# Kernel optimization log

Measured on AMD Instinct MI355X. Metric: run time of the kernel, lower is better.

Reference implementation:

```python
import jax, jax.numpy as jnp
import numpy as np

S, B, G, P = 8, 8192, 512, 16
E, H, BOT = 64, 64, 1024

def setup_inputs() -> dict:
    key = jax.random.key(0)
    k = jax.random.split(key, 9)
    in_xy = jax.random.normal(k[0], (S, B, 2), dtype=jnp.float32)
    in_dxdy = jax.random.normal(k[1], (S, B, 2), dtype=jnp.float32)
    h_states = jax.random.normal(k[2], (1, B, H), dtype=jnp.float32)
    starts = jnp.arange(G, dtype=jnp.int64) * P
    seq_start_end = jnp.stack([starts, starts + P], axis=1)
    W_emb = jax.random.normal(k[3], (2, E), dtype=jnp.float32) / jnp.sqrt(2.0)
    b_emb = jnp.zeros((E,), dtype=jnp.float32)
    W1 = jax.random.normal(k[4], (E + H, H), dtype=jnp.float32) / jnp.sqrt(float(E + H))
    b1 = jnp.zeros((H,), dtype=jnp.float32)
    W2 = jax.random.normal(k[5], (H, BOT), dtype=jnp.float32) / jnp.sqrt(float(H))
    b2 = jnp.zeros((BOT,), dtype=jnp.float32)
    return {"in_xy": in_xy, "in_dxdy": in_dxdy, "h_states": h_states,
            "seq_start_end": seq_start_end, "W_emb": W_emb, "b_emb": b_emb,
            "W1": W1, "b1": b1, "W2": W2, "b2": b2}

def reference(in_xy, in_dxdy, h_states, seq_start_end, W_emb, b_emb, W1, b1, W2, b2):
    # Uniform group size: P = batch / num_groups (groups are contiguous).
    batch = in_xy.shape[1]
    g = seq_start_end.shape[0]
    p = batch // g
    end_pos = in_xy[-1].reshape(g, p, 2)            # (G,P,2)
    h = h_states.reshape(batch, -1).reshape(g, p, -1)  # (G,P,H)
    # torch semantics: row (i*P+j) of the pair matrix uses pos[j]-pos[i], hidden[j]
    rel = end_pos[:, None, :, :] - end_pos[:, :, None, :]  # (G,P_i,P_j,2)
    emb = rel @ W_emb + b_emb                              # (G,P,P,E)
    hj = jnp.broadcast_to(h[:, None, :, :], (g, p, p, h.shape[-1]))
    x = jnp.concatenate([emb, hj], axis=-1)                # (G,P,P,E+H)
    x = jax.nn.relu(x @ W1 + b1)
    x = jax.nn.relu(x @ W2 + b2)                           # (G,P,P,BOT)
    pool = jnp.max(x, axis=2)                              # max over j -> (G,P,BOT)
    return pool.reshape(batch, -1)
```

## Files before the change

### kernel.cpp

```cpp
#include <hip/hip_runtime.h>
#include <hip/hip_bf16.h>

typedef __attribute__((ext_vector_type(8))) short bf16x8;
typedef __attribute__((ext_vector_type(4))) float f32x4;

#define NB 8192
#define NS 8

__device__ __forceinline__ unsigned short f2bf(float f) {
  union { float f; unsigned int u; } v; v.f = f;
  unsigned int r = v.u + 0x7FFFu + ((v.u >> 16) & 1u);
  return (unsigned short)(r >> 16);
}

__global__ __launch_bounds__(256) void prep_kernel(
    const float* __restrict__ W2, const float* __restrict__ W_emb,
    const float* __restrict__ b_emb, const float* __restrict__ W1,
    unsigned short* __restrict__ w2f, float* __restrict__ wc,
    unsigned short* __restrict__ w1bf) {
  int tid = blockIdx.x * 256 + threadIdx.x;
  if (tid < 8192) {
    int lane = tid & 63;
    int ks = (tid >> 6) & 1;
    int nt = tid >> 7;
    int col = nt * 16 + (lane & 15);
    int k0 = ks * 32 + (lane >> 4) * 8;
    bf16x8 pk;
#pragma unroll
    for (int e = 0; e < 8; ++e)
      pk[e] = (short)f2bf(W2[(k0 + e) * 1024 + col]);
    *(bf16x8*)(w2f + tid * 8) = pk;
  } else if (tid < 8192 + 192) {
    int t2 = tid - 8192;
    int c = t2 >> 6, k = t2 & 63;
    float s = 0.f;
    for (int e = 0; e < 64; ++e) {
      float src = (c < 2) ? W_emb[c * 64 + e] : b_emb[e];
      s += src * W1[e * 64 + k];
    }
    wc[t2] = s;
  } else if (tid < 8192 + 192 + 512) {
    int q = tid - 8384;
    int lane = q & 63;
    int fr = q >> 6;
    int nt = fr >> 1, ks = fr & 1;
    int col = nt * 16 + (lane & 15);
    int e0 = ks * 32 + (lane >> 4) * 8;
    bf16x8 pk;
#pragma unroll
    for (int e = 0; e < 8; ++e)
      pk[e] = (short)f2bf(W1[(64 + e0 + e) * 64 + col]);
    *(bf16x8*)(w1bf + q * 8) = pk;
  }
}

__global__ __launch_bounds__(64) void hw_kernel(
    const float* __restrict__ h_states, const float* __restrict__ b1,
    const float* __restrict__ wc, const unsigned short* __restrict__ w1bf,
    float* __restrict__ hW) {
  const int lane = threadIdx.x;
  const int b = blockIdx.x;
  const int row = b * 16 + (lane & 15);
  const int k0 = (lane >> 4) * 8;
  const float* hp = h_states + row * 64 + k0;
  bf16x8 a0, a1;
#pragma unroll
  for (int e = 0; e < 8; ++e) {
    a0[e] = (short)f2bf(hp[e]);
    a1[e] = (short)f2bf(hp[e + 32]);
  }
#pragma unroll
  for (int nt = 0; nt < 4; ++nt) {
    bf16x8 bf0 = *(const bf16x8*)(w1bf + ((nt * 2 + 0) * 64 + lane) * 8);
    bf16x8 bf1 = *(const bf16x8*)(w1bf + ((nt * 2 + 1) * 64 + lane) * 8);
    f32x4 z = {0.f, 0.f, 0.f, 0.f};
    f32x4 acc = __builtin_amdgcn_mfma_f32_16x16x32_bf16(a0, bf0, z, 0, 0, 0);
    acc = __builtin_amdgcn_mfma_f32_16x16x32_bf16(a1, bf1, acc, 0, 0, 0);
    int col = nt * 16 + (lane & 15);
    float bb = b1[col] + wc[128 + col];
#pragma unroll
    for (int r = 0; r < 4; ++r)
      hW[(b * 16 + (lane >> 4) * 4 + r) * 64 + col] = acc[r] + bb;
  }
}

__global__ __launch_bounds__(256, 4) void pool_kernel(
    const float* __restrict__ in_xy, const float* __restrict__ b2,
    const unsigned short* __restrict__ w2f, const float* __restrict__ wc,
    const float* __restrict__ hW, float* __restrict__ out) {
  __shared__ bf16x8 Afrag[2048];
  __shared__ float exy[32];
  const int g = blockIdx.x >> 1;
  const int half = blockIdx.x & 1;
  const int t = threadIdx.x;
  const int lane = t & 63;
  const int wv = t >> 6;

  if (t < 32) {
    int p = t & 15;
    exy[t] = in_xy[((NS - 1) * NB + g * 16 + p) * 2 + (t >> 4)];
  }

  float b2v[8];
#pragma unroll
  for (int u = 0; u < 8; ++u)
    b2v[u] = b2[half * 512 + wv * 128 + u * 16 + (lane & 15)];

  const int i = t & 15;
  const int kc = (t >> 4) & 3;
  const int ks = (t >> 6) & 1;
  const int k0 = ks * 32 + kc * 8;
  float w0[8], w1[8];
#pragma unroll
  for (int e = 0; e < 8; ++e) {
    w0[e] = wc[k0 + e];
    w1[e] = wc[64 + k0 + e];
  }
  __syncthreads();

  {
    float exi = exy[i], eyi = exy[16 + i];
#pragma unroll
    for (int c = 0; c < 8; ++c) {
      int j = (t >> 7) + 2 * c;
      float rx = exy[j] - exi;
      float ry = exy[16 + j] - eyi;
      const f32x4* hp = (const f32x4*)(hW + (g * 16 + j) * 64 + k0);
      f32x4 h0 = hp[0], h1 = hp[1];
      float hv[8] = {h0[0], h0[1], h0[2], h0[3], h1[0], h1[1], h1[2], h1[3]};
      bf16x8 pk;
#pragma unroll
      for (int e = 0; e < 8; ++e) {
        float v = fmaf(rx, w0[e], fmaf(ry, w1[e], hv[e]));
        v = fmaxf(v, 0.f);
        pk[e] = (short)f2bf(v);
      }
      Afrag[t + 256 * c] = pk;
    }
  }
  __syncthreads();

  const int rowbase = (g * 16 + (lane >> 4) * 4) * 1024 + half * 512 + wv * 128 + (lane & 15);
  const bf16x8* ap = Afrag + lane;
#pragma unroll
  for (int pass = 0; pass < 2; ++pass) {
    bf16x8 bfr[4][2];
#pragma unroll
    for (int u = 0; u < 4; ++u) {
      int nt = half * 32 + wv * 8 + pass * 4 + u;
      bfr[u][0] = *(const bf16x8*)(w2f + ((nt * 2 + 0) * 64 + lane) * 8);
      bfr[u][1] = *(const bf16x8*)(w2f + ((nt * 2 + 1) * 64 + lane) * 8);
    }
    f32x4 pool[4];
#pragma unroll
    for (int u = 0; u < 4; ++u) pool[u] = (f32x4){-3.4e38f, -3.4e38f, -3.4e38f, -3.4e38f};

#pragma unroll 4
    for (int j = 0; j < 16; ++j) {
      bf16x8 a0 = ap[j * 128];
      bf16x8 a1 = ap[j * 128 + 64];
      f32x4 acc[4];
      __builtin_amdgcn_s_setprio(1);
#pragma unroll
      for (int u = 0; u < 4; ++u) {
        f32x4 z = {0.f, 0.f, 0.f, 0.f};
        acc[u] = __builtin_amdgcn_mfma_f32_16x16x32_bf16(a0, bfr[u][0], z, 0, 0, 0);
      }
#pragma unroll
      for (int u = 0; u < 4; ++u)
        acc[u] = __builtin_amdgcn_mfma_f32_16x16x32_bf16(a1, bfr[u][1], acc[u], 0, 0, 0);
      __builtin_amdgcn_s_setprio(0);
#pragma unroll
      for (int u = 0; u < 4; ++u) {
#pragma unroll
        for (int r = 0; r < 4; ++r) pool[u][r] = fmaxf(pool[u][r], acc[u][r]);
      }
    }
#pragma unroll
    for (int u = 0; u < 4; ++u) {
      float bb = b2v[pass * 4 + u];
#pragma unroll
      for (int r = 0; r < 4; ++r)
        out[rowbase + r * 1024 + (pass * 4 + u) * 16] = fmaxf(pool[u][r] + bb, 0.f);
    }
  }
}

extern "C" void kernel_launch(void* const* d_in, const int* in_sizes, int n_in,
                              void* d_out, int out_size, void* d_ws, size_t ws_size,
                              hipStream_t stream) {
  const float* in_xy = (const float*)d_in[0];
  const float* h_states = (const float*)d_in[2];
  const float* W_emb = (const float*)d_in[4];
  const float* b_emb = (const float*)d_in[5];
  const float* W1 = (const float*)d_in[6];
  const float* b1 = (const float*)d_in[7];
  const float* W2 = (const float*)d_in[8];
  const float* b2 = (const float*)d_in[9];
  float* out = (float*)d_out;

  unsigned short* w2f = (unsigned short*)d_ws;
  float* wc = (float*)((char*)d_ws + 131072);
  unsigned short* w1bf = (unsigned short*)((char*)d_ws + 132096);
  float* hW = (float*)((char*)d_ws + 262144);

  prep_kernel<<<35, 256, 0, stream>>>(W2, W_emb, b_emb, W1, w2f, wc, w1bf);
  hw_kernel<<<512, 64, 0, stream>>>(h_states, b1, wc, w1bf, hW);
  pool_kernel<<<1024, 256, 0, stream>>>(in_xy, b2, w2f, wc, hW, out);
}
```

Baseline: 29.82 us.

## Fuse hidden-state projection into pool kernel and software-pipeline MFMA loop

Removes the separate hw_kernel launch. Each pool block now computes its group's h·W1 projection with MFMA into shared memory, so the hW round trip through global memory is gone. The main loop is restructured to ping-pong two accumulator sets, so the max-reduction of one j overlaps with the MFMAs of the next and the A fragments are prefetched ahead. In exchange, the projection is computed twice per group (once in each half block), and the kernel uses more registers and shared memory.

```diff
diff --git a/kernel.cpp b/kernel.cpp
--- a/kernel.cpp
+++ b/kernel.cpp
@@ -54,41 +54,13 @@
   }
 }
 
-__global__ __launch_bounds__(64) void hw_kernel(
-    const float* __restrict__ h_states, const float* __restrict__ b1,
-    const float* __restrict__ wc, const unsigned short* __restrict__ w1bf,
-    float* __restrict__ hW) {
-  const int lane = threadIdx.x;
-  const int b = blockIdx.x;
-  const int row = b * 16 + (lane & 15);
-  const int k0 = (lane >> 4) * 8;
-  const float* hp = h_states + row * 64 + k0;
-  bf16x8 a0, a1;
-#pragma unroll
-  for (int e = 0; e < 8; ++e) {
-    a0[e] = (short)f2bf(hp[e]);
-    a1[e] = (short)f2bf(hp[e + 32]);
-  }
-#pragma unroll
-  for (int nt = 0; nt < 4; ++nt) {
-    bf16x8 bf0 = *(const bf16x8*)(w1bf + ((nt * 2 + 0) * 64 + lane) * 8);
-    bf16x8 bf1 = *(const bf16x8*)(w1bf + ((nt * 2 + 1) * 64 + lane) * 8);
-    f32x4 z = {0.f, 0.f, 0.f, 0.f};
-    f32x4 acc = __builtin_amdgcn_mfma_f32_16x16x32_bf16(a0, bf0, z, 0, 0, 0);
-    acc = __builtin_amdgcn_mfma_f32_16x16x32_bf16(a1, bf1, acc, 0, 0, 0);
-    int col = nt * 16 + (lane & 15);
-    float bb = b1[col] + wc[128 + col];
-#pragma unroll
-    for (int r = 0; r < 4; ++r)
-      hW[(b * 16 + (lane >> 4) * 4 + r) * 64 + col] = acc[r] + bb;
-  }
-}
-
 __global__ __launch_bounds__(256, 4) void pool_kernel(
-    const float* __restrict__ in_xy, const float* __restrict__ b2,
+    const float* __restrict__ in_xy, const float* __restrict__ h_states,
+    const float* __restrict__ b1, const float* __restrict__ b2,
     const unsigned short* __restrict__ w2f, const float* __restrict__ wc,
-    const float* __restrict__ hW, float* __restrict__ out) {
+    const unsigned short* __restrict__ w1bf, float* __restrict__ out) {
   __shared__ bf16x8 Afrag[2048];
+  __shared__ float hWs[16][72];
   __shared__ float exy[32];
   const int g = blockIdx.x >> 1;
   const int half = blockIdx.x & 1;
@@ -101,15 +73,34 @@
     exy[t] = in_xy[((NS - 1) * NB + g * 16 + p) * 2 + (t >> 4)];
   }
 
+  {
+    const int row = g * 16 + (lane & 15);
+    const int e0 = (lane >> 4) * 8;
+    const float* hp = h_states + row * 64 + e0;
+    bf16x8 ha0, ha1;
+#pragma unroll
+    for (int e = 0; e < 8; ++e) {
+      ha0[e] = (short)f2bf(hp[e]);
+      ha1[e] = (short)f2bf(hp[e + 32]);
+    }
+    bf16x8 bf0 = *(const bf16x8*)(w1bf + ((wv * 2 + 0) * 64 + lane) * 8);
+    bf16x8 bf1 = *(const bf16x8*)(w1bf + ((wv * 2 + 1) * 64 + lane) * 8);
+    f32x4 z = {0.f, 0.f, 0.f, 0.f};
+    f32x4 acc = __builtin_amdgcn_mfma_f32_16x16x32_bf16(ha0, bf0, z, 0, 0, 0);
+    acc = __builtin_amdgcn_mfma_f32_16x16x32_bf16(ha1, bf1, acc, 0, 0, 0);
+    int col = wv * 16 + (lane & 15);
+    float bb = b1[col] + wc[128 + col];
+#pragma unroll
+    for (int r = 0; r < 4; ++r)
+      hWs[(lane >> 4) * 4 + r][col] = acc[r] + bb;
+  }
+
   float b2v[8];
 #pragma unroll
   for (int u = 0; u < 8; ++u)
     b2v[u] = b2[half * 512 + wv * 128 + u * 16 + (lane & 15)];
-
   const int i = t & 15;
-  const int kc = (t >> 4) & 3;
-  const int ks = (t >> 6) & 1;
-  const int k0 = ks * 32 + kc * 8;
+  const int k0 = ((t >> 6) & 1) * 32 + ((t >> 4) & 3) * 8;
   float w0[8], w1[8];
 #pragma unroll
   for (int e = 0; e < 8; ++e) {
@@ -125,8 +116,8 @@
       int j = (t >> 7) + 2 * c;
       float rx = exy[j] - exi;
       float ry = exy[16 + j] - eyi;
-      const f32x4* hp = (const f32x4*)(hW + (g * 16 + j) * 64 + k0);
-      f32x4 h0 = hp[0], h1 = hp[1];
+      const f32x4* hp2 = (const f32x4*)&hWs[j][k0];
+      f32x4 h0 = hp2[0], h1 = hp2[1];
       float hv[8] = {h0[0], h0[1], h0[2], h0[3], h1[0], h1[1], h1[2], h1[3]};
       bf16x8 pk;
 #pragma unroll
@@ -142,6 +133,7 @@
 
   const int rowbase = (g * 16 + (lane >> 4) * 4) * 1024 + half * 512 + wv * 128 + (lane & 15);
   const bf16x8* ap = Afrag + lane;
+  const f32x4 NEGINF = {-3.4e38f, -3.4e38f, -3.4e38f, -3.4e38f};
 #pragma unroll
   for (int pass = 0; pass < 2; ++pass) {
     bf16x8 bfr[4][2];
@@ -151,31 +143,55 @@
       bfr[u][0] = *(const bf16x8*)(w2f + ((nt * 2 + 0) * 64 + lane) * 8);
       bfr[u][1] = *(const bf16x8*)(w2f + ((nt * 2 + 1) * 64 + lane) * 8);
     }
-    f32x4 pool[4];
-#pragma unroll
-    for (int u = 0; u < 4; ++u) pool[u] = (f32x4){-3.4e38f, -3.4e38f, -3.4e38f, -3.4e38f};
-
-#pragma unroll 4
-    for (int j = 0; j < 16; ++j) {
-      bf16x8 a0 = ap[j * 128];
-      bf16x8 a1 = ap[j * 128 + 64];
-      f32x4 acc[4];
+    f32x4 pool[4], accB[4];
+#pragma unroll
+    for (int u = 0; u < 4; ++u) { pool[u] = NEGINF; accB[u] = NEGINF; }
+
+    bf16x8 a0 = ap[0];
+    bf16x8 a1 = ap[64];
+#pragma unroll
+    for (int jj = 0; jj < 16; jj += 2) {
+      f32x4 accA[4];
       __builtin_amdgcn_s_setprio(1);
 #pragma unroll
       for (int u = 0; u < 4; ++u) {
         f32x4 z = {0.f, 0.f, 0.f, 0.f};
-        acc[u] = __builtin_amdgcn_mfma_f32_16x16x32_bf16(a0, bfr[u][0], z, 0, 0, 0);
+        accA[u] = __builtin_amdgcn_mfma_f32_16x16x32_bf16(a0, bfr[u][0], z, 0, 0, 0);
       }
 #pragma unroll
       for (int u = 0; u < 4; ++u)
-        acc[u] = __builtin_amdgcn_mfma_f32_16x16x32_bf16(a1, bfr[u][1], acc[u], 0, 0, 0);
+        accA[u] = __builtin_amdgcn_mfma_f32_16x16x32_bf16(a1, bfr[u][1], accA[u], 0, 0, 0);
       __builtin_amdgcn_s_setprio(0);
+      bf16x8 c0 = ap[(jj + 1) * 128];
+      bf16x8 c1 = ap[(jj + 1) * 128 + 64];
+#pragma unroll
+      for (int u = 0; u < 4; ++u)
+#pragma unroll
+        for (int r = 0; r < 4; ++r) pool[u][r] = fmaxf(pool[u][r], accB[u][r]);
+
+      __builtin_amdgcn_s_setprio(1);
 #pragma unroll
       for (int u = 0; u < 4; ++u) {
-#pragma unroll
-        for (int r = 0; r < 4; ++r) pool[u][r] = fmaxf(pool[u][r], acc[u][r]);
+        f32x4 z = {0.f, 0.f, 0.f, 0.f};
+        accB[u] = __builtin_amdgcn_mfma_f32_16x16x32_bf16(c0, bfr[u][0], z, 0, 0, 0);
       }
-    }
+#pragma unroll
+      for (int u = 0; u < 4; ++u)
+        accB[u] = __builtin_amdgcn_mfma_f32_16x16x32_bf16(c1, bfr[u][1], accB[u], 0, 0, 0);
+      __builtin_amdgcn_s_setprio(0);
+      int jn = (jj + 2) & 15;
+      a0 = ap[jn * 128];
+      a1 = ap[jn * 128 + 64];
+#pragma unroll
+      for (int u = 0; u < 4; ++u)
+#pragma unroll
+        for (int r = 0; r < 4; ++r) pool[u][r] = fmaxf(pool[u][r], accA[u][r]);
+    }
+#pragma unroll
+    for (int u = 0; u < 4; ++u)
+#pragma unroll
+      for (int r = 0; r < 4; ++r) pool[u][r] = fmaxf(pool[u][r], accB[u][r]);
+
 #pragma unroll
     for (int u = 0; u < 4; ++u) {
       float bb = b2v[pass * 4 + u];
@@ -202,9 +218,7 @@
   unsigned short* w2f = (unsigned short*)d_ws;
   float* wc = (float*)((char*)d_ws + 131072);
   unsigned short* w1bf = (unsigned short*)((char*)d_ws + 132096);
-  float* hW = (float*)((char*)d_ws + 262144);
 
   prep_kernel<<<35, 256, 0, stream>>>(W2, W_emb, b_emb, W1, w2f, wc, w1bf);
-  hw_kernel<<<512, 64, 0, stream>>>(h_states, b1, wc, w1bf, hW);
-  pool_kernel<<<1024, 256, 0, stream>>>(in_xy, b2, w2f, wc, hW, out);
-}
+  pool_kernel<<<1024, 256, 0, stream>>>(in_xy, h_states, b1, b2, w2f, wc, w1bf, out);
+}
```

Measured after the change: 28.23 us. -5.4%, faster.
